# Optimization experiments

Measured on AMD Instinct MI355X. Metric: run time of the kernel, lower is better.

## Reference

```python
import jax, jax.numpy as jnp
import numpy as np

NUM_HEADS = 16
HEAD_DIM = 256  # hidden_size // num_heads = 4096 // 16
SEQ = 240       # hardcoded in the original forward's view(1, 240, -1)
IN_SIZE = 4096
HID = 4096


def setup_inputs() -> dict:
    key = jax.random.key(0)
    ks = jax.random.split(key, 10)
    s = 0.02
    return {
        "input1": jax.random.normal(ks[0], (SEQ, IN_SIZE), jnp.float32),
        "input2": jax.random.normal(ks[1], (SEQ, IN_SIZE), jnp.float32),
        "Wq": jax.random.normal(ks[2], (HID, IN_SIZE), jnp.float32) * s,
        "bq": jax.random.normal(ks[3], (HID,), jnp.float32) * s,
        "Wk": jax.random.normal(ks[4], (HID, IN_SIZE), jnp.float32) * s,
        "bk": jax.random.normal(ks[5], (HID,), jnp.float32) * s,
        "Wv": jax.random.normal(ks[6], (HID, IN_SIZE), jnp.float32) * s,
        "bv": jax.random.normal(ks[7], (HID,), jnp.float32) * s,
    }


def reference(input1, input2, Wq, bq, Wk, bk, Wv, bv):
    # QKV projections (torch Linear: x @ W^T + b)
    q = input1 @ Wq.T + bq  # [S, HID]
    k = input2 @ Wk.T + bk
    v = input2 @ Wv.T + bv
    # [1, H, S, hd]
    q = q.reshape(1, SEQ, NUM_HEADS, HEAD_DIM).transpose(0, 2, 1, 3)
    k = k.reshape(1, SEQ, NUM_HEADS, HEAD_DIM).transpose(0, 2, 1, 3)
    v = v.reshape(1, SEQ, NUM_HEADS, HEAD_DIM).transpose(0, 2, 1, 3)
    scores = jnp.einsum("bhqd,bhkd->bhqk", q, k) / jnp.sqrt(jnp.float32(HEAD_DIM))
    w = jax.nn.softmax(scores, axis=-1)  # [1, H, Sq, Sk]
    # NOTE: the original does attention_weights.transpose(-2,-1) @ value, i.e. attn^T @ V
    out = jnp.einsum("bhqk,bhqd->bhkd", w, v)  # [1, H, Sk, hd]
    out = out.transpose(0, 2, 1, 3).reshape(1, SEQ, HID)
    # linear_out exists in __init__ but is never applied in forward.
    return out
```

## Files before the change

### kernel.cpp

```cpp
#include <hip/hip_runtime.h>
#include <hip/hip_bf16.h>

#define SEQ 240
#define HID 4096
#define NH 16
#define HD 256

typedef float f32x4 __attribute__((ext_vector_type(4)));
typedef short s16x8 __attribute__((ext_vector_type(8)));
typedef short s16x4 __attribute__((ext_vector_type(4)));

__device__ __forceinline__ short f2bf(float f) {
    unsigned u = __builtin_bit_cast(unsigned, f);
    unsigned r = u + 0x7FFFu + ((u >> 16) & 1u);
    return (short)(r >> 16);
}

__device__ __forceinline__ s16x8 cvt8(float4 a, float4 b) {
    s16x8 r;
    r[0] = f2bf(a.x); r[1] = f2bf(a.y); r[2] = f2bf(a.z); r[3] = f2bf(a.w);
    r[4] = f2bf(b.x); r[5] = f2bf(b.y); r[6] = f2bf(b.z); r[7] = f2bf(b.w);
    return r;
}

__device__ __forceinline__ s16x8 cvtpk8(f32x4 a, f32x4 b) {
    union { unsigned u[4]; s16x8 s; } r;
    asm("v_cvt_pk_bf16_f32 %0, %1, %2" : "=v"(r.u[0]) : "v"(a[0]), "v"(a[1]));
    asm("v_cvt_pk_bf16_f32 %0, %1, %2" : "=v"(r.u[1]) : "v"(a[2]), "v"(a[3]));
    asm("v_cvt_pk_bf16_f32 %0, %1, %2" : "=v"(r.u[2]) : "v"(b[0]), "v"(b[1]));
    asm("v_cvt_pk_bf16_f32 %0, %1, %2" : "=v"(r.u[3]) : "v"(b[2]), "v"(b[3]));
    return r.s;
}

__device__ __forceinline__ void dma16(const void* g, void* l) {
    __builtin_amdgcn_global_load_lds(
        (const __attribute__((address_space(1))) unsigned int*)g,
        (__attribute__((address_space(3))) unsigned int*)l,
        16, 0, 0);
}

__global__ __launch_bounds__(256) void cvt_kernel(
    const float* __restrict__ in1, const float* __restrict__ in2,
    short* __restrict__ A1, short* __restrict__ A2)
{
    const int i = blockIdx.x * 256 + threadIdx.x;
    const float* __restrict__ src = blockIdx.y ? in2 : in1;
    short* __restrict__ dst = blockIdx.y ? A2 : A1;
    const int r = i >> 9;
    const int c = (i & 511) * 8;
    s16x8 v = (s16x8){0,0,0,0,0,0,0,0};
    if (r < SEQ) {
        float4 a = *(const float4*)&src[(size_t)r * HID + c];
        float4 b = *(const float4*)&src[(size_t)r * HID + c + 4];
        v = cvt8(a, b);
    }
    *(s16x8*)&dst[(size_t)r * HID + c] = v;
}

__global__ __launch_bounds__(256, 3) void qkv_gemm(
    const short* __restrict__ A1, const short* __restrict__ A2,
    const float* __restrict__ Wq, const float* __restrict__ Wk,
    const float* __restrict__ Wv,
    float* __restrict__ pqk, float* __restrict__ pvt, int KC)
{
    const int g  = blockIdx.y;
    const int z  = blockIdx.z;
    const int nb = blockIdx.x * 64;
    const short* __restrict__ A = (g == 0) ? A1 : A2;
    const float* __restrict__ W = (g == 0) ? Wq : (g == 1) ? Wk : Wv;

    const int tid  = threadIdx.x;
    const int lane = tid & 63;
    const int w    = tid >> 6;
    const int lr   = lane & 15;
    const int lg   = lane >> 4;

    __shared__ short As[2][256 * 32];
    __shared__ float Bs[2][64 * 32];

    f32x4 acc[4][4];
    #pragma unroll
    for (int m = 0; m < 4; ++m)
        #pragma unroll
        for (int n = 0; n < 4; ++n)
            acc[m][n] = (f32x4){0.f, 0.f, 0.f, 0.f};

    const short* gA[4];
    #pragma unroll
    for (int j = 0; j < 4; ++j) {
        const int row = (j * 4 + w) * 16 + (lane >> 2);
        const int c   = (lane & 3) ^ ((row >> 1) & 3);
        gA[j] = A + (size_t)row * HID + (size_t)z * KC + c * 8;
    }
    const float* gW[2];
    #pragma unroll
    for (int j = 0; j < 2; ++j) {
        const int row = (j * 4 + w) * 8 + (lane >> 3);
        const int c   = (lane & 7) ^ (row & 7);
        gW[j] = W + (size_t)(nb + row) * HID + (size_t)z * KC + c * 4;
    }

    int aoff[4];
    #pragma unroll
    for (int m = 0; m < 4; ++m) {
        const int row = w * 64 + m * 16 + lr;
        aoff[m] = row * 32 + ((lg ^ ((row >> 1) & 3)) * 8);
    }
    int boff0[4], boff1[4];
    #pragma unroll
    for (int n = 0; n < 4; ++n) {
        const int row = n * 16 + lr;
        boff0[n] = row * 32 + (((2 * lg)     ^ (row & 7)) * 4);
        boff1[n] = row * 32 + (((2 * lg + 1) ^ (row & 7)) * 4);
    }

#define ISSUE(bb) {                                                          \
    _Pragma("unroll")                                                        \
    for (int j = 0; j < 4; ++j) {                                            \
        dma16(gA[j], &As[bb][(j * 4 + w) * 512]);  gA[j] += 32; }            \
    _Pragma("unroll")                                                        \
    for (int j = 0; j < 2; ++j) {                                            \
        dma16(gW[j], &Bs[bb][(j * 4 + w) * 256]);  gW[j] += 32; } }

    ISSUE(0)
    ISSUE(1)
    asm volatile("s_waitcnt vmcnt(6)" ::: "memory");
    __builtin_amdgcn_s_barrier();
    __builtin_amdgcn_sched_barrier(0);

    const int NIT = KC / 32;
    for (int t = 0; t < NIT; ++t) {
        const int b = t & 1;

        s16x8 af[4], bf[4];
        #pragma unroll
        for (int m = 0; m < 4; ++m)
            af[m] = *(const s16x8*)&As[b][aoff[m]];
        #pragma unroll
        for (int n = 0; n < 4; ++n) {
            f32x4 x0 = *(const f32x4*)&Bs[b][boff0[n]];
            f32x4 x1 = *(const f32x4*)&Bs[b][boff1[n]];
            bf[n] = cvtpk8(x0, x1);
        }
        #pragma unroll
        for (int m = 0; m < 4; ++m)
            #pragma unroll
            for (int n = 0; n < 4; ++n)
                acc[m][n] = __builtin_amdgcn_mfma_f32_16x16x32_bf16(af[m], bf[n], acc[m][n], 0, 0, 0);

        if (t + 1 < NIT) {
            asm volatile("s_waitcnt lgkmcnt(0)" ::: "memory");
            __builtin_amdgcn_s_barrier();
            __builtin_amdgcn_sched_barrier(0);
            if (t + 2 < NIT) {
                ISSUE(b)
                asm volatile("s_waitcnt vmcnt(6)" ::: "memory");
            } else {
                asm volatile("s_waitcnt vmcnt(0)" ::: "memory");
            }
            __builtin_amdgcn_s_barrier();
            __builtin_amdgcn_sched_barrier(0);
        }
    }
#undef ISSUE

    if (g == 2) {
        float* pout = pvt + (size_t)z * HID * SEQ;
        #pragma unroll
        for (int m = 0; m < 4; ++m) {
            const int row0 = w * 64 + m * 16 + lg * 4;
            if (row0 >= SEQ) continue;
            #pragma unroll
            for (int n = 0; n < 4; ++n) {
                const int col = nb + n * 16 + lr;
                float4 o = make_float4(acc[m][n][0], acc[m][n][1], acc[m][n][2], acc[m][n][3]);
                *(float4*)&pout[(size_t)col * SEQ + row0] = o;
            }
        }
    } else {
        float* pout = pqk + (size_t)(z * 2 + g) * SEQ * HID;
        #pragma unroll
        for (int m = 0; m < 4; ++m) {
            const int row0 = w * 64 + m * 16 + lg * 4;
            if (row0 >= SEQ) continue;
            #pragma unroll
            for (int n = 0; n < 4; ++n) {
                const int col = nb + n * 16 + lr;
                #pragma unroll
                for (int r = 0; r < 4; ++r)
                    pout[(size_t)(row0 + r) * HID + col] = acc[m][n][r];
            }
        }
    }
}

__global__ __launch_bounds__(256) void reduce_qk(
    const float* __restrict__ pqk,
    const float* __restrict__ bq, const float* __restrict__ bk,
    short* __restrict__ qb, short* __restrict__ kb, int KS)
{
    const int g   = blockIdx.y;
    const int idx = blockIdx.x * 256 + threadIdx.x;
    f32x4 s = (f32x4){0.f, 0.f, 0.f, 0.f};
    for (int z = 0; z < KS; ++z)
        s += *(const f32x4*)&pqk[(size_t)(z * 2 + g) * SEQ * HID + (size_t)idx * 4];
    const int n = (idx * 4) & (HID - 1);
    const float* bias = g ? bk : bq;
    s += *(const f32x4*)&bias[n];
    short* ob = g ? kb : qb;
    s16x4 o = (s16x4){f2bf(s[0]), f2bf(s[1]), f2bf(s[2]), f2bf(s[3])};
    *(s16x4*)&ob[(size_t)idx * 4] = o;
}

__global__ __launch_bounds__(256) void reduce_v(
    const float* __restrict__ pvt, const float* __restrict__ bv,
    short* __restrict__ vtb, int KS)
{
    const int idx = blockIdx.x * 256 + threadIdx.x;
    f32x4 s = (f32x4){0.f, 0.f, 0.f, 0.f};
    for (int z = 0; z < KS; ++z)
        s += *(const f32x4*)&pvt[(size_t)z * HID * SEQ + (size_t)idx * 4];
    const int n = idx / 60;
    const float b = bv[n];
    s16x4 o = (s16x4){f2bf(s[0] + b), f2bf(s[1] + b), f2bf(s[2] + b), f2bf(s[3] + b)};
    *(s16x4*)&vtb[(size_t)idx * 4] = o;
}

__global__ __launch_bounds__(256) void scores_kernel(
    const short* __restrict__ qb, const short* __restrict__ kb,
    short* __restrict__ ptb)
{
    const int it   = blockIdx.x;
    const int h    = blockIdx.y;
    const int tid  = threadIdx.x;
    const int lane = tid & 63;
    const int w    = tid >> 6;
    const int lr   = lane & 15;
    const int lg   = lane >> 4;
    const int jt0  = w * 4;
    const int NJT  = (w < 3) ? 4 : 3;

    __shared__ float redmax[4][16];
    __shared__ float redsum[4][16];

    f32x4 acc[4];
    #pragma unroll
    for (int j = 0; j < 4; ++j) acc[j] = (f32x4){0.f, 0.f, 0.f, 0.f};

    const int ib = it * 16;
    const short* qrow = &qb[(size_t)(ib + lr) * HID + h * HD + lg * 8];

    for (int d0 = 0; d0 < HD; d0 += 32) {
        s16x8 afr = *(const s16x8*)&qrow[d0];
        #pragma unroll
        for (int j = 0; j < 4; ++j) {
            if (j < NJT) {
                s16x8 bfr = *(const s16x8*)&kb[(size_t)((jt0 + j) * 16 + lr) * HID + h * HD + d0 + lg * 8];
                acc[j] = __builtin_amdgcn_mfma_f32_16x16x32_bf16(afr, bfr, acc[j], 0, 0, 0);
            }
        }
    }

    const float sc = 0.0625f;
    #pragma unroll
    for (int j = 0; j < 4; ++j) acc[j] *= sc;

    #pragma unroll
    for (int r = 0; r < 4; ++r) {
        float mx = -1e30f;
        #pragma unroll
        for (int j = 0; j < 4; ++j) if (j < NJT) mx = fmaxf(mx, acc[j][r]);
        #pragma unroll
        for (int s = 1; s < 16; s <<= 1) mx = fmaxf(mx, __shfl_xor(mx, s, 64));
        if (lr == 0) redmax[w][lg * 4 + r] = mx;
    }
    __syncthreads();
    #pragma unroll
    for (int r = 0; r < 4; ++r) {
        const int i = lg * 4 + r;
        float mx = fmaxf(fmaxf(redmax[0][i], redmax[1][i]),
                         fmaxf(redmax[2][i], redmax[3][i]));
        float sum = 0.f;
        #pragma unroll
        for (int j = 0; j < 4; ++j) {
            if (j < NJT) {
                float e = expf(acc[j][r] - mx);
                acc[j][r] = e;
                sum += e;
            }
        }
        #pragma unroll
        for (int s = 1; s < 16; s <<= 1) sum += __shfl_xor(sum, s, 64);
        if (lr == 0) redsum[w][i] = sum;
    }
    __syncthreads();
    #pragma unroll
    for (int r = 0; r < 4; ++r) {
        const int i = lg * 4 + r;
        const float inv = 1.f / (redsum[0][i] + redsum[1][i] + redsum[2][i] + redsum[3][i]);
        #pragma unroll
        for (int j = 0; j < 4; ++j) if (j < NJT) acc[j][r] *= inv;
    }
    #pragma unroll
    for (int j = 0; j < 4; ++j) {
        if (j < NJT) {
            const int jj = (jt0 + j) * 16 + lr;
            s16x4 o = (s16x4){f2bf(acc[j][0]), f2bf(acc[j][1]), f2bf(acc[j][2]), f2bf(acc[j][3])};
            *(s16x4*)&ptb[(size_t)(h * SEQ + jj) * SEQ + ib + lg * 4] = o;
        }
    }
}

__global__ __launch_bounds__(256) void pv_kernel(
    const short* __restrict__ ptb, const short* __restrict__ vtb,
    float* __restrict__ out)
{
    const int dt   = blockIdx.x;
    const int h    = blockIdx.y;
    const int tid  = threadIdx.x;
    const int lane = tid & 63;
    const int w    = tid >> 6;
    const int lr   = lane & 15;
    const int lg   = lane >> 4;
    const int NJT  = (w < 3) ? 4 : 3;

    f32x4 acc[4];
    #pragma unroll
    for (int j = 0; j < 4; ++j) acc[j] = (f32x4){0.f, 0.f, 0.f, 0.f};

    const short* vrow = &vtb[(size_t)(h * HD + dt * 16 + lr) * SEQ + lg * 8];

    for (int i0 = 0; i0 < 256; i0 += 32) {
        const bool ok = (i0 + lg * 8) < SEQ;
        s16x8 bfr = (s16x8){0,0,0,0,0,0,0,0};
        if (ok) bfr = *(const s16x8*)&vrow[i0];
        #pragma unroll
        for (int j = 0; j < 4; ++j) {
            if (j < NJT) {
                const int jt = w + j * 4;
                s16x8 afr = (s16x8){0,0,0,0,0,0,0,0};
                if (ok) afr = *(const s16x8*)&ptb[(size_t)(h * SEQ + jt * 16 + lr) * SEQ + i0 + lg * 8];
                acc[j] = __builtin_amdgcn_mfma_f32_16x16x32_bf16(afr, bfr, acc[j], 0, 0, 0);
            }
        }
    }

    #pragma unroll
    for (int j = 0; j < 4; ++j) {
        if (j < NJT) {
            const int jt = w + j * 4;
            #pragma unroll
            for (int r = 0; r < 4; ++r)
                out[(size_t)(jt * 16 + lg * 4 + r) * HID + h * HD + dt * 16 + lr] = acc[j][r];
        }
    }
}

extern "C" void kernel_launch(void* const* d_in, const int* in_sizes, int n_in,
                              void* d_out, int out_size, void* d_ws, size_t ws_size,
                              hipStream_t stream) {
    const float* in1 = (const float*)d_in[0];
    const float* in2 = (const float*)d_in[1];
    const float* Wq  = (const float*)d_in[2];
    const float* bq  = (const float*)d_in[3];
    const float* Wk  = (const float*)d_in[4];
    const float* bk  = (const float*)d_in[5];
    const float* Wv  = (const float*)d_in[6];
    const float* bv  = (const float*)d_in[7];
    float* out = (float*)d_out;

    char* w = (char*)d_ws;
    short* A1  = (short*)w;  w += (size_t)256 * HID * 2;
    short* A2  = (short*)w;  w += (size_t)256 * HID * 2;
    short* qb  = (short*)w;  w += (size_t)SEQ * HID * 2;
    short* kb  = (short*)w;  w += (size_t)SEQ * HID * 2;
    short* vtb = (short*)w;  w += (size_t)HID * SEQ * 2;
    short* ptb = (short*)w;  w += (size_t)NH * SEQ * SEQ * 2;
    float* pqk = (float*)w;
    const size_t fixed  = (size_t)(w - (char*)d_ws);
    const size_t perKS  = ((size_t)2 * SEQ * HID + (size_t)HID * SEQ) * sizeof(float);

    int KS = 1;
    if (fixed + 4 * perKS <= ws_size)      KS = 4;
    else if (fixed + 2 * perKS <= ws_size) KS = 2;
    const int KC = HID / KS;
    float* pvt = pqk + (size_t)KS * 2 * SEQ * HID;

    cvt_kernel<<<dim3(512, 2), 256, 0, stream>>>(in1, in2, A1, A2);
    qkv_gemm<<<dim3(64, 3, KS), 256, 0, stream>>>(A1, A2, Wq, Wk, Wv, pqk, pvt, KC);
    reduce_qk<<<dim3(960, 2), 256, 0, stream>>>(pqk, bq, bk, qb, kb, KS);
    reduce_v<<<960, 256, 0, stream>>>(pvt, bv, vtb, KS);
    scores_kernel<<<dim3(15, 16), 256, 0, stream>>>(qb, kb, ptb);
    pv_kernel<<<dim3(16, 16), 256, 0, stream>>>(ptb, vtb, out);
}
```

Measured before the change: 106.5 us.

## Load activation fragments directly to registers and deepen W tile to K=128

The QKV GEMM no longer stages the bf16 activation tile through LDS. Each wave loads its A fragments straight from global memory into double-buffered registers, prefetching the next K-slice during compute. The fp32 weight tile in LDS grows from K=32 to K=128 per stage, which cuts barriers and loop iterations by four. The cost is many more VGPRs (32 s16x8 fragment registers), so occupancy drops from 3 to 2 blocks per launch bound, and the vmcnt accounting becomes more intricate.

```diff
diff --git a/kernel.cpp b/kernel.cpp
--- a/kernel.cpp
+++ b/kernel.cpp
@@ -57,7 +57,7 @@
     *(s16x8*)&dst[(size_t)r * HID + c] = v;
 }
 
-__global__ __launch_bounds__(256, 3) void qkv_gemm(
+__global__ __launch_bounds__(256, 2) void qkv_gemm(
     const short* __restrict__ A1, const short* __restrict__ A2,
     const float* __restrict__ Wq, const float* __restrict__ Wk,
     const float* __restrict__ Wv,
@@ -75,8 +75,7 @@
     const int lr   = lane & 15;
     const int lg   = lane >> 4;
 
-    __shared__ short As[2][256 * 32];
-    __shared__ float Bs[2][64 * 32];
+    __shared__ float Bs[2][64 * 128];
 
     f32x4 acc[4][4];
     #pragma unroll
@@ -85,84 +84,86 @@
         for (int n = 0; n < 4; ++n)
             acc[m][n] = (f32x4){0.f, 0.f, 0.f, 0.f};
 
-    const short* gA[4];
-    #pragma unroll
-    for (int j = 0; j < 4; ++j) {
-        const int row = (j * 4 + w) * 16 + (lane >> 2);
-        const int c   = (lane & 3) ^ ((row >> 1) & 3);
-        gA[j] = A + (size_t)row * HID + (size_t)z * KC + c * 8;
-    }
-    const float* gW[2];
-    #pragma unroll
-    for (int j = 0; j < 2; ++j) {
-        const int row = (j * 4 + w) * 8 + (lane >> 3);
-        const int c   = (lane & 7) ^ (row & 7);
-        gW[j] = W + (size_t)(nb + row) * HID + (size_t)z * KC + c * 4;
-    }
-
-    int aoff[4];
-    #pragma unroll
-    for (int m = 0; m < 4; ++m) {
-        const int row = w * 64 + m * 16 + lr;
-        aoff[m] = row * 32 + ((lg ^ ((row >> 1) & 3)) * 8);
-    }
-    int boff0[4], boff1[4];
-    #pragma unroll
-    for (int n = 0; n < 4; ++n) {
-        const int row = n * 16 + lr;
-        boff0[n] = row * 32 + (((2 * lg)     ^ (row & 7)) * 4);
-        boff1[n] = row * 32 + (((2 * lg + 1) ^ (row & 7)) * 4);
-    }
-
-#define ISSUE(bb) {                                                          \
-    _Pragma("unroll")                                                        \
-    for (int j = 0; j < 4; ++j) {                                            \
-        dma16(gA[j], &As[bb][(j * 4 + w) * 512]);  gA[j] += 32; }            \
-    _Pragma("unroll")                                                        \
-    for (int j = 0; j < 2; ++j) {                                            \
-        dma16(gW[j], &Bs[bb][(j * 4 + w) * 256]);  gW[j] += 32; } }
+    const float* gW[8];
+    #pragma unroll
+    for (int j = 0; j < 8; ++j) {
+        const int p   = w * 8 + j;
+        const int row = 2 * p + (lane >> 5);
+        const int sl  = (lane & 31) ^ (row & 7);
+        gW[j] = W + (size_t)(nb + row) * HID + (size_t)z * KC + sl * 4;
+    }
+
+    const short* __restrict__ ap = A + (size_t)(w * 64 + lr) * HID + (size_t)z * KC + lg * 8;
+
+    int boff0[4][4], boff1[4][4];
+    #pragma unroll
+    for (int n = 0; n < 4; ++n)
+        #pragma unroll
+        for (int ks = 0; ks < 4; ++ks) {
+            const int row = n * 16 + lr;
+            const int sg  = ks * 8 + lg * 2;
+            boff0[n][ks] = row * 128 + (((sg    ) ^ (row & 7)) << 2);
+            boff1[n][ks] = row * 128 + (((sg + 1) ^ (row & 7)) << 2);
+        }
+
+#define ISSUE(bb) { _Pragma("unroll")                                        \
+    for (int j = 0; j < 8; ++j) {                                            \
+        dma16(gW[j], &Bs[bb][(w * 8 + j) * 256]);  gW[j] += 128; } }
+
+#define LOAD_AF(dst, kk) { _Pragma("unroll")                                 \
+    for (int m = 0; m < 4; ++m) { _Pragma("unroll")                          \
+      for (int ks = 0; ks < 4; ++ks)                                         \
+        dst[m*4+ks] = *(const s16x8*)(ap + (size_t)m * 16 * HID + (kk) + ks * 32); } }
+
+    s16x8 afA[16], afB[16];
 
     ISSUE(0)
     ISSUE(1)
-    asm volatile("s_waitcnt vmcnt(6)" ::: "memory");
+    LOAD_AF(afA, 0)
+    asm volatile("s_waitcnt vmcnt(24)" ::: "memory");
     __builtin_amdgcn_s_barrier();
     __builtin_amdgcn_sched_barrier(0);
 
-    const int NIT = KC / 32;
+    const int NIT = KC / 128;
     for (int t = 0; t < NIT; ++t) {
         const int b = t & 1;
-
-        s16x8 af[4], bf[4];
-        #pragma unroll
-        for (int m = 0; m < 4; ++m)
-            af[m] = *(const s16x8*)&As[b][aoff[m]];
-        #pragma unroll
-        for (int n = 0; n < 4; ++n) {
-            f32x4 x0 = *(const f32x4*)&Bs[b][boff0[n]];
-            f32x4 x1 = *(const f32x4*)&Bs[b][boff1[n]];
-            bf[n] = cvtpk8(x0, x1);
-        }
-        #pragma unroll
-        for (int m = 0; m < 4; ++m)
-            #pragma unroll
-            for (int n = 0; n < 4; ++n)
-                acc[m][n] = __builtin_amdgcn_mfma_f32_16x16x32_bf16(af[m], bf[n], acc[m][n], 0, 0, 0);
+        const s16x8* af = (t & 1) ? afB : afA;
+
+        #pragma unroll
+        for (int ks = 0; ks < 4; ++ks) {
+            s16x8 bf[4];
+            #pragma unroll
+            for (int n = 0; n < 4; ++n) {
+                f32x4 x0 = *(const f32x4*)&Bs[b][boff0[n][ks]];
+                f32x4 x1 = *(const f32x4*)&Bs[b][boff1[n][ks]];
+                bf[n] = cvtpk8(x0, x1);
+            }
+            #pragma unroll
+            for (int m = 0; m < 4; ++m)
+                #pragma unroll
+                for (int n = 0; n < 4; ++n)
+                    acc[m][n] = __builtin_amdgcn_mfma_f32_16x16x32_bf16(af[m*4+ks], bf[n], acc[m][n], 0, 0, 0);
+        }
 
         if (t + 1 < NIT) {
+            if (t & 1) { LOAD_AF(afA, (t + 1) * 128) }
+            else       { LOAD_AF(afB, (t + 1) * 128) }
+            __builtin_amdgcn_sched_barrier(0);
             asm volatile("s_waitcnt lgkmcnt(0)" ::: "memory");
             __builtin_amdgcn_s_barrier();
             __builtin_amdgcn_sched_barrier(0);
             if (t + 2 < NIT) {
                 ISSUE(b)
-                asm volatile("s_waitcnt vmcnt(6)" ::: "memory");
+                asm volatile("s_waitcnt vmcnt(24)" ::: "memory");
             } else {
-                asm volatile("s_waitcnt vmcnt(0)" ::: "memory");
+                asm volatile("s_waitcnt vmcnt(16)" ::: "memory");
             }
             __builtin_amdgcn_s_barrier();
             __builtin_amdgcn_sched_barrier(0);
         }
     }
 #undef ISSUE
+#undef LOAD_AF
 
     if (g == 2) {
         float* pout = pvt + (size_t)z * HID * SEQ;
```

Result: slower. 189.9 us (+78.4%).
